# Performance work log

Hardware: AMD Instinct MI355X
Metric: run time of the kernel (lower is better)

The kernel has to match this reference:

```python
import jax, jax.numpy as jnp
import numpy as np

S, B, H, L = 1024, 128, 1024, 2
D = 2 * H  # concat dim: hidden + input (input_size == hidden_size)


def setup_inputs() -> dict:
    key = jax.random.key(0)
    k1, k2, k3 = jax.random.split(key, 3)
    inputs = jax.random.normal(k1, (S, B, H), dtype=jnp.float32)
    lim = 1.0 / np.sqrt(D)  # torch Linear default init range
    W = jax.random.uniform(k2, (L, 4, D), jnp.float32, -lim, lim)  # rows: i, c~, f, o
    b = jax.random.uniform(k3, (L, 4), jnp.float32, -lim, lim)
    return {"inputs": inputs, "W": W, "b": b}


def _lstm(inputs, W, b):
    Ln = W.shape[0]
    Bn, Hd = inputs.shape[1], inputs.shape[2]
    h0 = jnp.zeros((Ln, Bn, Hd), inputs.dtype)
    c0 = jnp.zeros_like(h0)

    def step(carry, x_t):
        h, c = carry  # each [L, B, H]
        inp = x_t     # [B, H]
        hs, cs = [], []
        for l in range(Ln):
            z = jnp.concatenate([h[l], inp], axis=-1)  # [B, 2H], order [H_t_1, X_t]
            g = z @ W[l].T + b[l]                       # [B, 4] — four 1-out Linears fused
            i_t = jax.nn.sigmoid(g[:, 0:1])
            c_hat = jnp.tanh(g[:, 1:2])
            f_t = jax.nn.sigmoid(g[:, 2:3])
            o_t = jax.nn.sigmoid(g[:, 3:4])
            c_new = f_t * c[l] + i_t * c_hat            # scalar gates broadcast over [B, H]
            h_new = o_t * jnp.tanh(c_new)
            hs.append(h_new)
            cs.append(c_new)
            inp = h_new
        h = jnp.stack(hs)
        c = jnp.stack(cs)
        return (h, c), h[-1]

    (hT, cT), outs = jax.lax.scan(step, (h0, c0), inputs)
    return outs, hT, cT  # outs: [S, B, H]


def reference(inputs, W, b):
    outs, hT, cT = _lstm(inputs, W, b)
    return (outs, (hT, cT))
```

## Files before the change

### kernel.cpp

```cpp
#include <hip/hip_runtime.h>

#define SS 1024
#define BB 128
#define HH 1024
#define LL 2
#define DD 2048
#define NROWS (SS*BB)
#define TSEG 512
#define NSEG 2
#define ROWSEG (TSEG*BB)
#define RPW 8
#define NSCANB 16
#define NWORKB 2048
#define L2E  1.4426950408889634f

typedef float f32x4 __attribute__((ext_vector_type(4)));

__device__ __forceinline__ float fast_rcp(float x)  { return __builtin_amdgcn_rcpf(x); }
__device__ __forceinline__ float exp2_(float x)     { return __builtin_amdgcn_exp2f(x); }

template<int CTRL>
__device__ __forceinline__ float qperm(float x){
    return __int_as_float(__builtin_amdgcn_update_dpp(0, __float_as_int(x), CTRL, 0xF, 0xF, true));
}
__device__ __forceinline__ float rowshr4(float x){
    return __int_as_float(__builtin_amdgcn_update_dpp(0, __float_as_int(x), 0x114, 0xF, 0xF, true));
}

__global__ __launch_bounds__(256) void fused_phase(
    const float* __restrict__ x, const float* __restrict__ W,
    const float* __restrict__ bias, float* out,
    float* __restrict__ s_out, float* __restrict__ finals,
    float* __restrict__ sums, float* __restrict__ state,
    int s1, int s2, int s3, int fin)
{
    float* pre = out + (size_t)NROWS * HH;
    const int tid = threadIdx.x;

    if (blockIdx.x < NSCANB) {
        if (tid >= 64) return;
        const int lane = tid;

        if (s2 < 0) {
            if (blockIdx.x == 0 && s1 == 0) {
                for (int s = 0; s < 12; ++s) {
                    const int base = (s < 4) ? s*DD
                                   : (s < 8) ? 4*DD + (s-4)*DD
                                             : 4*DD + (s-8)*DD + HH;
                    float v = 0.f;
                    #pragma unroll
                    for (int k = 0; k < 16; ++k) v += W[base + lane + k*64];
                    #pragma unroll
                    for (int off = 32; off >= 1; off >>= 1) v += __shfl_xor(v, off, 64);
                    if (lane == 0) sums[s] = v;
                }
            }
            return;
        }

        const int gate = lane & 3;
        const int L    = (lane >> 2) & 1;
        const int lb   = lane >> 3;
        const int bb   = blockIdx.x * 8 + lb;

        const float sh = sums[L*4 + gate];
        const float sx = sums[8 + gate];
        const float sc  = (gate == 1) ? (2.0f*L2E) : (-L2E);
        const float s_h = sh * sc;
        const float sxc = L ? sx * sc : 0.0f;
        const float pcc = L ? bias[4+gate] * sc : 0.0f;
        const float Ac  = (gate == 1) ? 1.0f : 0.0f;
        const float Bc  = (gate == 0) ? (2.0f*L2E) : ((gate == 1) ? -2.0f : 1.0f);

        const float* pbase = pre + ((size_t)bb << 12) + gate;
        float* so = s_out + (size_t)bb * SS;

        const int t_lo = s2 * TSEG, t_hi = t_lo + TSEG;

        float h, cp, h0d1, h0d2;
        float4* st = (float4*)state + blockIdx.x*64 + lane;
        if (t_lo == 0) { h = 0.f; cp = 0.f; h0d1 = 0.f; h0d2 = 0.f; }
        else { float4 s = *st; h = s.x; cp = s.y; h0d1 = s.z; h0d2 = s.w; }

        float hb0 = 0.f, hb1 = 0.f, hb2 = 0.f, hb3 = 0.f;

        __builtin_amdgcn_s_setprio(3);

        float buf[64];
        for (int ch = 0; ch < TSEG/64; ++ch) {
            const int tc = t_lo + ch*64;
            #pragma unroll
            for (int uu = 0; uu < 64; ++uu)
                buf[uu] = pbase[(size_t)(tc + uu) * 4];
            #pragma unroll
            for (int uu = 0; uu < 64; ++uu) {
                const float p = L ? pcc : buf[uu];
                const float P = fmaf(h0d2, sxc, p);
                const float g = fmaf(h, s_h, P);
                const float v = fmaf(Bc, fast_rcp(1.0f + exp2_(g)), Ac);
                const float w = v * qperm<0xB1>(v);
                const float cpn = fmaf(qperm<0xAA>(v), cp, qperm<0x00>(w));
                const float th = fmaf(-2.0f, fast_rcp(1.0f + exp2_(cpn)), 1.0f);
                const float hn = qperm<0xFF>(v) * th;
                const bool disc = (ch == 0) && (uu < 2) && L;
                h  = disc ? h  : hn;
                cp = disc ? cp : cpn;
                h0d2 = h0d1;
                h0d1 = rowshr4(h);

                if (((uu+2)&3)==0) hb0 = h;
                else if (((uu+2)&3)==1) hb1 = h;
                else if (((uu+2)&3)==2) hb2 = h;
                else hb3 = h;
                if (((uu&3)==1) && (ch > 0 || uu >= 5) && L && gate == 0) {
                    *(float4*)(so + tc + uu - 5) = make_float4(hb0,hb1,hb2,hb3);
                }
            }
        }

        const float h0f = h, c0f = cp;

        #pragma unroll
        for (int fs = 0; fs < 2; ++fs) {
            const float p = L ? pcc : buf[63];
            const float P = fmaf(h0d2, sxc, p);
            const float g = fmaf(h, s_h, P);
            const float v = fmaf(Bc, fast_rcp(1.0f + exp2_(g)), Ac);
            const float w = v * qperm<0xB1>(v);
            const float cpn = fmaf(qperm<0xAA>(v), cp, qperm<0x00>(w));
            const float th = fmaf(-2.0f, fast_rcp(1.0f + exp2_(cpn)), 1.0f);
            const float hn = qperm<0xFF>(v) * th;
            if (L) { h = hn; cp = cpn;
                     if (fs == 0) hb2 = hn; else hb3 = hn; }
            h0d2 = h0d1;
        }
        if (L && gate == 0)
            *(float4*)(so + t_hi - 4) = make_float4(hb0,hb1,hb2,hb3);

        __builtin_amdgcn_s_setprio(0);

        *st = make_float4(h, cp, h0d1, h0d2);

        if (t_hi == SS && gate == 0) {
            if (L) { finals[128+bb] = h;   finals[384+bb] = cp  * (0.5f/L2E); }
            else   { finals[bb]     = h0f; finals[256+bb] = c0f * (0.5f/L2E); }
        }
        return;
    }

    const int lane = tid & 63;
    const int gw   = (blockIdx.x - NSCANB)*4 + (tid >> 6);

    if (s1 >= 0) {
        float4 wv[4][4];
        #pragma unroll
        for (int j = 0; j < 4; ++j)
            #pragma unroll
            for (int it = 0; it < 4; ++it)
                wv[j][it] = *(const float4*)(W + j*DD + HH + it*256 + lane*4);
        const float4 b0 = *(const float4*)(bias);

        #pragma unroll 2
        for (int j = 0; j < RPW; ++j) {
            const int row = s1*ROWSEG + gw*RPW + j;
            const float* xr = x + (size_t)row * HH;
            float a0 = 0.f, a1 = 0.f, a2 = 0.f, a3 = 0.f;
            #pragma unroll
            for (int it = 0; it < 4; ++it) {
                f32x4 xv = __builtin_nontemporal_load((const f32x4*)xr + it*64 + lane);
                a0 = fmaf(xv.x, wv[0][it].x, fmaf(xv.y, wv[0][it].y, fmaf(xv.z, wv[0][it].z, fmaf(xv.w, wv[0][it].w, a0))));
                a1 = fmaf(xv.x, wv[1][it].x, fmaf(xv.y, wv[1][it].y, fmaf(xv.z, wv[1][it].z, fmaf(xv.w, wv[1][it].w, a1))));
                a2 = fmaf(xv.x, wv[2][it].x, fmaf(xv.y, wv[2][it].y, fmaf(xv.z, wv[2][it].z, fmaf(xv.w, wv[2][it].w, a2))));
                a3 = fmaf(xv.x, wv[3][it].x, fmaf(xv.y, wv[3][it].y, fmaf(xv.z, wv[3][it].z, fmaf(xv.w, wv[3][it].w, a3))));
            }
            #pragma unroll
            for (int off = 32; off >= 1; off >>= 1) {
                a0 += __shfl_xor(a0, off, 64);
                a1 += __shfl_xor(a1, off, 64);
                a2 += __shfl_xor(a2, off, 64);
                a3 += __shfl_xor(a3, off, 64);
            }
            if (lane == 0) {
                float4 r = make_float4((a0 + b0.x) * (-L2E),
                                       (a1 + b0.y) * ( 2.0f * L2E),
                                       (a2 + b0.z) * (-L2E),
                                       (a3 + b0.w) * (-L2E));
                const int b = row & (BB-1), t = row >> 7;
                *(float4*)(pre + (((size_t)b << 10) + t) * 4) = r;
            }
        }
    }

    if (s3 >= 0) {
        #pragma unroll
        for (int rep = 0; rep < 2; ++rep) {
            const int g  = gw*2 + rep;
            const int b  = g >> 7;
            const int t0 = s3*TSEG + (g & 127)*4;
            float4 v4 = *(const float4*)(s_out + (size_t)b*SS + t0);
            #pragma unroll
            for (int jj = 0; jj < 4; ++jj) {
                const float vb = (jj==0) ? v4.x : (jj==1) ? v4.y : (jj==2) ? v4.z : v4.w;
                const f32x4 vv = {vb, vb, vb, vb};
                f32x4* dst = (f32x4*)(out + ((size_t)(t0+jj)*BB + b) * HH);
                #pragma unroll
                for (int it = 0; it < 4; ++it)
                    __builtin_nontemporal_store(vv, dst + it*64 + lane);
            }
        }
    }

    if (fin && gw < 512) {
        const float v = finals[gw];
        const f32x4 vv = {v, v, v, v};
        f32x4* dst = (f32x4*)(out + (size_t)(NROWS + gw) * HH);
        #pragma unroll
        for (int it = 0; it < 4; ++it)
            __builtin_nontemporal_store(vv, dst + it*64 + lane);
    }
}

extern "C" void kernel_launch(void* const* d_in, const int* in_sizes, int n_in,
                              void* d_out, int out_size, void* d_ws, size_t ws_size,
                              hipStream_t stream) {
    const float* x    = (const float*)d_in[0];
    const float* W    = (const float*)d_in[1];
    const float* bias = (const float*)d_in[2];
    float* out = (float*)d_out;

    float* s_out  = (float*)d_ws;
    float* finals = s_out + NROWS;
    float* sums   = finals + 512;
    float* state  = sums + 16;

    for (int p = 0; p < 4; ++p) {
        const int a1 = (p <= 1) ? p : -1;
        const int a2 = (p >= 1 && p <= 2) ? p - 1 : -1;
        const int a3 = (p >= 2) ? p - 2 : -1;
        const int fn = (p == 3) ? 1 : 0;
        hipLaunchKernelGGL(fused_phase, dim3(NSCANB + NWORKB), dim3(256), 0, stream,
                           x, W, bias, out, s_out, finals, sums, state,
                           a1, a2, a3, fn);
    }
}
```

Measured before the change: 236.8 us.

## Interleave four independent batch chains per scan wave to hide recurrence latency

Each scan wave now carries four independent batch groups (32 batches per block), with their serial recurrence steps interleaved. This gives instruction-level parallelism to cover the latency of the exp/rcp/DPP dependency chain. The number of scan blocks drops from 16 to 4 and the prefetch chunk shrinks from 64 to 16 steps. In exchange the kernel uses more registers and fewer waves for the scan, and loads are issued in smaller batches.

```diff
diff --git a/kernel.cpp b/kernel.cpp
--- a/kernel.cpp
+++ b/kernel.cpp
@@ -10,7 +10,7 @@
 #define NSEG 2
 #define ROWSEG (TSEG*BB)
 #define RPW 8
-#define NSCANB 16
+#define NSCANB 4
 #define NWORKB 2048
 #define L2E  1.4426950408889634f
 
@@ -61,7 +61,7 @@
         const int gate = lane & 3;
         const int L    = (lane >> 2) & 1;
         const int lb   = lane >> 3;
-        const int bb   = blockIdx.x * 8 + lb;
+        const int sw   = blockIdx.x;
 
         const float sh = sums[L*4 + gate];
         const float sx = sums[8 + gate];
@@ -72,78 +72,104 @@
         const float Ac  = (gate == 1) ? 1.0f : 0.0f;
         const float Bc  = (gate == 0) ? (2.0f*L2E) : ((gate == 1) ? -2.0f : 1.0f);
 
-        const float* pbase = pre + ((size_t)bb << 12) + gate;
-        float* so = s_out + (size_t)bb * SS;
+        const float* pb[4];
+        float* so[4];
+        #pragma unroll
+        for (int c = 0; c < 4; ++c) {
+            const int bb = sw*32 + c*8 + lb;
+            pb[c] = pre + ((size_t)bb << 12) + gate;
+            so[c] = s_out + (size_t)bb * SS;
+        }
 
         const int t_lo = s2 * TSEG, t_hi = t_lo + TSEG;
 
-        float h, cp, h0d1, h0d2;
-        float4* st = (float4*)state + blockIdx.x*64 + lane;
-        if (t_lo == 0) { h = 0.f; cp = 0.f; h0d1 = 0.f; h0d2 = 0.f; }
-        else { float4 s = *st; h = s.x; cp = s.y; h0d1 = s.z; h0d2 = s.w; }
-
-        float hb0 = 0.f, hb1 = 0.f, hb2 = 0.f, hb3 = 0.f;
+        float h[4], cp[4], d1[4], d2[4], hb[4][4];
+        #pragma unroll
+        for (int c = 0; c < 4; ++c) {
+            float4* st = (float4*)state + (sw*4 + c)*64 + lane;
+            if (t_lo == 0) { h[c]=0.f; cp[c]=0.f; d1[c]=0.f; d2[c]=0.f; }
+            else { float4 s = *st; h[c]=s.x; cp[c]=s.y; d1[c]=s.z; d2[c]=s.w; }
+            hb[c][0]=0.f; hb[c][1]=0.f; hb[c][2]=0.f; hb[c][3]=0.f;
+        }
 
         __builtin_amdgcn_s_setprio(3);
 
-        float buf[64];
-        for (int ch = 0; ch < TSEG/64; ++ch) {
-            const int tc = t_lo + ch*64;
-            #pragma unroll
-            for (int uu = 0; uu < 64; ++uu)
-                buf[uu] = pbase[(size_t)(tc + uu) * 4];
-            #pragma unroll
-            for (int uu = 0; uu < 64; ++uu) {
-                const float p = L ? pcc : buf[uu];
-                const float P = fmaf(h0d2, sxc, p);
-                const float g = fmaf(h, s_h, P);
+        float buf[4][16];
+        for (int ch = 0; ch < TSEG/16; ++ch) {
+            const int tc = t_lo + ch*16;
+            #pragma unroll
+            for (int c = 0; c < 4; ++c)
+                #pragma unroll
+                for (int uu = 0; uu < 16; ++uu)
+                    buf[c][uu] = pb[c][(size_t)(tc + uu) * 4];
+            #pragma unroll
+            for (int uu = 0; uu < 16; ++uu) {
+                #pragma unroll
+                for (int c = 0; c < 4; ++c) {
+                    const float p = L ? pcc : buf[c][uu];
+                    const float P = fmaf(d2[c], sxc, p);
+                    const float g = fmaf(h[c], s_h, P);
+                    const float v = fmaf(Bc, fast_rcp(1.0f + exp2_(g)), Ac);
+                    const float w = v * qperm<0xB1>(v);
+                    const float cpn = fmaf(qperm<0xAA>(v), cp[c], qperm<0x00>(w));
+                    const float th = fmaf(-2.0f, fast_rcp(1.0f + exp2_(cpn)), 1.0f);
+                    const float hn = qperm<0xFF>(v) * th;
+                    const bool disc = (ch == 0) && (uu < 2) && L;
+                    h[c]  = disc ? h[c]  : hn;
+                    cp[c] = disc ? cp[c] : cpn;
+                    d2[c] = d1[c];
+                    d1[c] = rowshr4(h[c]);
+                    hb[c][(uu+2)&3] = h[c];
+                    if (((uu&3)==1) && (ch > 0 || uu >= 5) && L && gate == 0)
+                        *(float4*)(so[c] + tc + uu - 5)
+                            = make_float4(hb[c][0],hb[c][1],hb[c][2],hb[c][3]);
+                }
+            }
+        }
+
+        float h0f[4], c0f[4];
+        #pragma unroll
+        for (int c = 0; c < 4; ++c) { h0f[c] = h[c]; c0f[c] = cp[c]; }
+
+        #pragma unroll
+        for (int fs = 0; fs < 2; ++fs) {
+            #pragma unroll
+            for (int c = 0; c < 4; ++c) {
+                const float p = pcc;
+                const float P = fmaf(d2[c], sxc, p);
+                const float g = fmaf(h[c], s_h, P);
                 const float v = fmaf(Bc, fast_rcp(1.0f + exp2_(g)), Ac);
                 const float w = v * qperm<0xB1>(v);
-                const float cpn = fmaf(qperm<0xAA>(v), cp, qperm<0x00>(w));
+                const float cpn = fmaf(qperm<0xAA>(v), cp[c], qperm<0x00>(w));
                 const float th = fmaf(-2.0f, fast_rcp(1.0f + exp2_(cpn)), 1.0f);
                 const float hn = qperm<0xFF>(v) * th;
-                const bool disc = (ch == 0) && (uu < 2) && L;
-                h  = disc ? h  : hn;
-                cp = disc ? cp : cpn;
-                h0d2 = h0d1;
-                h0d1 = rowshr4(h);
-
-                if (((uu+2)&3)==0) hb0 = h;
-                else if (((uu+2)&3)==1) hb1 = h;
-                else if (((uu+2)&3)==2) hb2 = h;
-                else hb3 = h;
-                if (((uu&3)==1) && (ch > 0 || uu >= 5) && L && gate == 0) {
-                    *(float4*)(so + tc + uu - 5) = make_float4(hb0,hb1,hb2,hb3);
-                }
-            }
-        }
-
-        const float h0f = h, c0f = cp;
-
-        #pragma unroll
-        for (int fs = 0; fs < 2; ++fs) {
-            const float p = L ? pcc : buf[63];
-            const float P = fmaf(h0d2, sxc, p);
-            const float g = fmaf(h, s_h, P);
-            const float v = fmaf(Bc, fast_rcp(1.0f + exp2_(g)), Ac);
-            const float w = v * qperm<0xB1>(v);
-            const float cpn = fmaf(qperm<0xAA>(v), cp, qperm<0x00>(w));
-            const float th = fmaf(-2.0f, fast_rcp(1.0f + exp2_(cpn)), 1.0f);
-            const float hn = qperm<0xFF>(v) * th;
-            if (L) { h = hn; cp = cpn;
-                     if (fs == 0) hb2 = hn; else hb3 = hn; }
-            h0d2 = h0d1;
-        }
-        if (L && gate == 0)
-            *(float4*)(so + t_hi - 4) = make_float4(hb0,hb1,hb2,hb3);
+                if (L) { h[c] = hn; cp[c] = cpn;
+                         if (fs == 0) hb[c][2] = hn; else hb[c][3] = hn; }
+                d2[c] = d1[c];
+            }
+        }
+        if (L && gate == 0) {
+            #pragma unroll
+            for (int c = 0; c < 4; ++c)
+                *(float4*)(so[c] + t_hi - 4)
+                    = make_float4(hb[c][0],hb[c][1],hb[c][2],hb[c][3]);
+        }
 
         __builtin_amdgcn_s_setprio(0);
 
-        *st = make_float4(h, cp, h0d1, h0d2);
+        #pragma unroll
+        for (int c = 0; c < 4; ++c) {
+            float4* st = (float4*)state + (sw*4 + c)*64 + lane;
+            *st = make_float4(h[c], cp[c], d1[c], d2[c]);
+        }
 
         if (t_hi == SS && gate == 0) {
-            if (L) { finals[128+bb] = h;   finals[384+bb] = cp  * (0.5f/L2E); }
-            else   { finals[bb]     = h0f; finals[256+bb] = c0f * (0.5f/L2E); }
+            #pragma unroll
+            for (int c = 0; c < 4; ++c) {
+                const int bb = sw*32 + c*8 + lb;
+                if (L) { finals[128+bb] = h[c];   finals[384+bb] = cp[c]  * (0.5f/L2E); }
+                else   { finals[bb]     = h0f[c]; finals[256+bb] = c0f[c] * (0.5f/L2E); }
+            }
         }
         return;
     }
```

New measurement: 388.9 us. 1.64x slower.
